# Kernel tuning notes

Measured on AMD Instinct MI355X. Metric: run time of the kernel, lower is better.

## Reference

```python
import jax, jax.numpy as jnp
import numpy as np
import math


def setup_inputs() -> dict:
    key = jax.random.key(0)
    k1, k2 = jax.random.split(key)
    N, FEATS, K = 100000, 256, 2000
    node_embs = jax.random.normal(k1, (N, FEATS), dtype=jnp.float32)
    # mask of zeros = all nodes valid (original uses -inf for invalid nodes)
    mask = jnp.zeros((N, 1), dtype=jnp.float32)
    # scorer param, uniform(-stdv, stdv) with stdv = 1/sqrt(feats), as in reset_param
    stdv = 1.0 / math.sqrt(FEATS)
    scorer = jax.random.uniform(k2, (FEATS, 1), minval=-stdv, maxval=stdv, dtype=jnp.float32)
    return {"node_embs": node_embs, "mask": mask, "scorer": scorer, "k": K}


def reference(node_embs, mask, scorer, k):
    # scores: [N,1] = (node_embs @ scorer) / sum(scorer) + mask
    scores = (node_embs @ scorer) / jnp.sum(scorer) + mask
    # top-k over flattened scores (column dim is 1, so indices == node indices)
    vals, topk_indices = jax.lax.top_k(scores.ravel(), k)
    # NOTE: original filters vals > -inf (drops masked-out picks); with a finite
    # (all-zeros) mask every selected entry passes, so shape stays static [k].
    out = jnp.take(node_embs, topk_indices, axis=0)  # [k, feats]
    return out.T  # [feats, k]
```

## Files before the change

### kernel.cpp

```cpp
#include <hip/hip_runtime.h>
#include <stdint.h>


#define NBINS 4096
#define BIN_SHIFT 20
#define CAP 4096
#define HPARTS 8

__device__ __forceinline__ uint32_t f2key(float f) {
  uint32_t b = __float_as_uint(f);
  return (b & 0x80000000u) ? ~b : (b | 0x80000000u);
}

__global__ __launch_bounds__(256) void k1_scores(
    const float* __restrict__ embs, const float* __restrict__ mask,
    const float* __restrict__ scorer, uint32_t* __restrict__ keys,
    uint32_t* __restrict__ hdr, uint32_t* __restrict__ hist, int N) {
  __shared__ float tile[32 * 132];
  __shared__ float sw[256];
  __shared__ float Ssh;
  int t = threadIdx.x;
  int r0 = blockIdx.x * 32;
  if (blockIdx.x == 0) {
    if (t < 16) hdr[t] = 0u;
    for (int i = t; i < NBINS; i += 256) hist[i] = 0u;
  }
  sw[t] = scorer[t];
  __syncthreads();
  if (t < 64) {
    double s = 0.0;
    for (int j = t; j < 256; j += 64) s += (double)sw[j];
#pragma unroll
    for (int off = 32; off >= 1; off >>= 1) s += __shfl_xor(s, off, 64);
    if (t == 0) Ssh = (float)s;
  }
  __syncthreads();
  float S = Ssh;
  int r = t >> 3, c = t & 7;
  float acc = 0.f;
  const float4* e4 = (const float4*)embs;
#pragma unroll
  for (int ch = 0; ch < 2; ++ch) {
    if (ch) __syncthreads();
#pragma unroll
    for (int m = 0; m < 4; ++m) {
      int flat = m * 256 + t;
      int rr = flat >> 5;
      int cc4 = flat & 31;
      int row = r0 + rr;
      float4 v = make_float4(0.f, 0.f, 0.f, 0.f);
      if (row < N) v = e4[(size_t)row * 64 + ch * 32 + cc4];
      float* dst = &tile[rr * 132 + cc4 * 4];
      dst[0] = v.x; dst[1] = v.y; dst[2] = v.z; dst[3] = v.w;
    }
    __syncthreads();
#pragma unroll
    for (int sl = 0; sl < 16; ++sl) {
      acc = fmaf(tile[r * 132 + c + 8 * sl], sw[ch * 128 + c + 8 * sl], acc);
    }
  }
  float m1 = acc + __shfl_xor(acc, 4, 64);
  float p1 = m1 + __shfl_xor(m1, 1, 64);
  float dot = p1 + __shfl_xor(p1, 2, 64);
  int row = r0 + r;
  if (c == 0 && row < N) {
    float score = dot / S + mask[row];
    keys[row] = f2key(score);
  }
}

__global__ __launch_bounds__(1024) void kHistFind(
    const uint32_t* __restrict__ keys, uint32_t* __restrict__ hist,
    uint32_t* __restrict__ hdr, int N, int k) {
  __shared__ uint32_t h[2][NBINS];
  __shared__ uint32_t wtot[16], wsuf[16];
  int t = threadIdx.x, bid = blockIdx.x;
  int lane = t & 63, wave = t >> 6;

  for (int i = t; i < 2 * NBINS; i += 1024) ((uint32_t*)h)[i] = 0u;
  __syncthreads();
  int per = (N + HPARTS - 1) / HPARTS;
  int lo = bid * per;
  int hi = lo + per; if (hi > N) hi = N;
  int sub = (t >> 7) & 1;
  int n4 = (hi - lo) >> 2;
  const uint4* q4 = (const uint4*)(keys + lo);
  for (int i = t; i < n4; i += 1024) {
    uint4 v = q4[i];
    atomicAdd(&h[sub][v.x >> BIN_SHIFT], 1u);
    atomicAdd(&h[sub][v.y >> BIN_SHIFT], 1u);
    atomicAdd(&h[sub][v.z >> BIN_SHIFT], 1u);
    atomicAdd(&h[sub][v.w >> BIN_SHIFT], 1u);
  }
  for (int i = lo + (n4 << 2) + t; i < hi; i += 1024)
    atomicAdd(&h[sub][keys[i] >> BIN_SHIFT], 1u);
  __syncthreads();
  for (int i = t; i < NBINS; i += 1024) {
    uint32_t v = h[0][i] + h[1][i];
    if (v) atomicAdd(&hist[i], v);
  }
  __syncthreads();
  if (t == 0) {
    __threadfence();
    __hip_atomic_fetch_add(&hdr[8], 1u, __ATOMIC_ACQ_REL, __HIP_MEMORY_SCOPE_AGENT);
  }
  if (bid != 0) return;

  if (t == 0) {
    while (__hip_atomic_load(&hdr[8], __ATOMIC_RELAXED, __HIP_MEMORY_SCOPE_AGENT) < HPARTS)
      __builtin_amdgcn_s_sleep(8);
    (void)__hip_atomic_load(&hdr[8], __ATOMIC_ACQUIRE, __HIP_MEMORY_SCOPE_AGENT);
  }
  __syncthreads();

  uint4 a = ((const uint4*)hist)[t];
  uint32_t rb[4] = {a.x, a.y, a.z, a.w};
  uint32_t p4 = rb[0] + rb[1] + rb[2] + rb[3];
  uint32_t x = p4;
#pragma unroll
  for (int off = 1; off < 64; off <<= 1) {
    uint32_t v = __shfl_down(x, off, 64);
    if (lane + off < 64) x += v;
  }
  if (lane == 0) wtot[wave] = x;
  __syncthreads();
  if (t < 16) {
    uint32_t y = wtot[t];
#pragma unroll
    for (int off = 1; off < 16; off <<= 1) {
      uint32_t v = __shfl_down(y, off, 64);
      if (t + off < 16) y += v;
    }
    wsuf[t] = y - wtot[t];
  }
  __syncthreads();
  uint32_t St = x + wsuf[wave];
  uint32_t above = St - p4;
  if (above < (uint32_t)k && St >= (uint32_t)k) {
    uint32_t cum = above;
#pragma unroll
    for (int jj = 3; jj >= 0; --jj) {
      if (cum + rb[jj] >= (uint32_t)k) { hdr[0] = (uint32_t)(t * 4 + jj); hdr[1] = cum; break; }
      cum += rb[jj];
    }
  }
}

__global__ __launch_bounds__(256) void k3_compact(
    const uint32_t* __restrict__ keys, const uint32_t* __restrict__ hdr,
    uint32_t* __restrict__ ckey, uint32_t* __restrict__ cidx,
    uint32_t* __restrict__ counter, int N) {
  __shared__ uint32_t wcnt[4];
  __shared__ uint32_t wbase[4];
  __shared__ uint32_t blkbase;
  int i = blockIdx.x * 256 + threadIdx.x;
  int wave = threadIdx.x >> 6, lane = threadIdx.x & 63;
  uint32_t B = hdr[0];
  bool pred = false;
  uint32_t key = 0;
  if (i < N) {
    key = keys[i];
    pred = (key >> BIN_SHIFT) >= B;
  }
  unsigned long long ball = __ballot(pred);
  uint32_t prefix = (uint32_t)__popcll(ball & ((1ull << lane) - 1ull));
  if (lane == 0) wcnt[wave] = (uint32_t)__popcll(ball);
  __syncthreads();
  if (threadIdx.x == 0) {
    uint32_t tot = wcnt[0] + wcnt[1] + wcnt[2] + wcnt[3];
    blkbase = tot ? atomicAdd(counter, tot) : 0u;
    wbase[0] = 0;
    wbase[1] = wcnt[0];
    wbase[2] = wcnt[0] + wcnt[1];
    wbase[3] = wcnt[0] + wcnt[1] + wcnt[2];
  }
  __syncthreads();
  if (pred) {
    uint32_t pos = blkbase + wbase[wave] + prefix;
    if (pos < CAP) { ckey[pos] = key; cidx[pos] = (uint32_t)i; }
  }
}

__global__ __launch_bounds__(256) void k4_rank(
    const uint32_t* __restrict__ ckey, const uint32_t* __restrict__ cidx,
    const uint32_t* __restrict__ hdr, uint32_t* __restrict__ oidx, int k) {
  __shared__ uint32_t lk[CAP];
  __shared__ uint32_t li[CAP];
  uint32_t C = hdr[2];
  if (C > CAP) C = CAP;
  uint32_t base = blockIdx.x * 16u;
  if (base >= C) return;
  for (uint32_t j = threadIdx.x; j < C; j += 256u) {
    lk[j] = ckey[j];
    li[j] = cidx[j];
  }
  __syncthreads();
  int wave = threadIdx.x >> 6, lane = threadIdx.x & 63;
  uint32_t g0 = base + wave * 4u;
  uint32_t mk[4], mi[4], cnt[4];
#pragma unroll
  for (int q = 0; q < 4; ++q) {
    uint32_t g = g0 + q;
    bool valid = g < C;
    mk[q] = valid ? lk[g] : 0u;
    mi[q] = valid ? li[g] : 0xFFFFFFFFu;
    cnt[q] = 0u;
  }
  for (uint32_t j = lane; j < C; j += 64u) {
    uint32_t kj = lk[j], ij = li[j];
#pragma unroll
    for (int q = 0; q < 4; ++q)
      cnt[q] += (kj > mk[q] || (kj == mk[q] && ij < mi[q])) ? 1u : 0u;
  }
#pragma unroll
  for (int q = 0; q < 4; ++q) {
#pragma unroll
    for (int off = 32; off >= 1; off >>= 1) cnt[q] += __shfl_xor(cnt[q], off, 64);
  }
  if (lane == 0) {
#pragma unroll
    for (int q = 0; q < 4; ++q) {
      uint32_t g = g0 + q;
      if (g < C && cnt[q] < (uint32_t)k) oidx[cnt[q]] = mi[q];
    }
  }
}

__global__ __launch_bounds__(256) void k5_gather(
    const float* __restrict__ embs, const uint32_t* __restrict__ oidx,
    float* __restrict__ out, int k) {
  __shared__ float tile[16 * 132];
  __shared__ uint32_t sidx[16];
  int t = threadIdx.x;
  int r0 = blockIdx.x * 16;
  int fb = blockIdx.y * 128;
  if (t < 16) sidx[t] = (r0 + t < k) ? oidx[r0 + t] : 0u;
  __syncthreads();
  const float4* e4 = (const float4*)embs;
#pragma unroll
  for (int m = 0; m < 2; ++m) {
    int flat = m * 256 + t;
    int rr = flat >> 5;
    int cc4 = flat & 31;
    float4 v = e4[(size_t)sidx[rr] * 64 + (fb >> 2) + cc4];
    float* dst = &tile[rr * 132 + cc4 * 4];
    dst[0] = v.x; dst[1] = v.y; dst[2] = v.z; dst[3] = v.w;
  }
  __syncthreads();
  int fl = t >> 1;
  int rq = t & 1;
  float v[8];
#pragma unroll
  for (int i = 0; i < 8; ++i) v[i] = tile[(rq * 8 + i) * 132 + fl];
  size_t obase = (size_t)(fb + fl) * k + r0 + rq * 8;
  if (((k & 3) == 0) && (r0 + rq * 8 + 7 < k)) {
    *(float4*)(out + obase) = make_float4(v[0], v[1], v[2], v[3]);
    *(float4*)(out + obase + 4) = make_float4(v[4], v[5], v[6], v[7]);
  } else {
#pragma unroll
    for (int i = 0; i < 8; ++i)
      if (r0 + rq * 8 + i < k) out[obase + i] = v[i];
  }
}

extern "C" void kernel_launch(void* const* d_in, const int* in_sizes, int n_in,
                              void* d_out, int out_size, void* d_ws, size_t ws_size,
                              hipStream_t stream) {
  const float* embs = (const float*)d_in[0];
  const float* mask = (const float*)d_in[1];
  const float* scorer = (const float*)d_in[2];
  int F = in_sizes[2];
  int N = in_sizes[0] / F;
  int k = out_size / F;

  uint32_t* keys = (uint32_t*)d_out;

  char* ws = (char*)d_ws;
  uint32_t* hdr = (uint32_t*)ws;
  uint32_t* hist = (uint32_t*)(ws + 1024);
  uint32_t* ckey = (uint32_t*)(ws + 1024 + NBINS * 4);
  uint32_t* cidx = ckey + CAP;
  uint32_t* oidx = cidx + CAP;

  k1_scores<<<(N + 31) / 32, 256, 0, stream>>>(embs, mask, scorer, keys, hdr, hist, N);
  kHistFind<<<HPARTS, 1024, 0, stream>>>(keys, hist, hdr, N, k);
  k3_compact<<<(N + 255) / 256, 256, 0, stream>>>(keys, hdr, ckey, cidx, &hdr[2], N);
  k4_rank<<<(CAP + 15) / 16, 256, 0, stream>>>(ckey, cidx, hdr, oidx, k);
  k5_gather<<<dim3((k + 15) / 16, 2), 256, 0, stream>>>(embs, oidx, (float*)d_out, k);
}
```

Before: 45.23 us.

## Fuse histogram/threshold kernel with compaction using grid-wide spin flag

Merges the histogram+threshold-find kernel and the compaction kernel into one launch of about 98 blocks of 1024 threads. The first 8 blocks build the histogram, block 0 finds the threshold bin and publishes it through an atomic flag, and all other blocks spin-wait on that flag before compacting their slice. This removes one kernel launch and its launch gap. It relies on every block being co-resident, otherwise spinning blocks could deadlock, and hdr[9] must be reset each call.

Result: faster. 43.28 us (median of 2 runs) (-4.3%).

```diff
diff --git a/kernel.cpp b/kernel.cpp
--- a/kernel.cpp
+++ b/kernel.cpp
@@ -69,93 +69,103 @@
   }
 }
 
-__global__ __launch_bounds__(1024) void kHistFind(
+__global__ __launch_bounds__(1024) void kSel(
     const uint32_t* __restrict__ keys, uint32_t* __restrict__ hist,
-    uint32_t* __restrict__ hdr, int N, int k) {
+    uint32_t* __restrict__ hdr, uint32_t* __restrict__ ckey,
+    uint32_t* __restrict__ cidx, int N, int k) {
   __shared__ uint32_t h[2][NBINS];
   __shared__ uint32_t wtot[16], wsuf[16];
+  __shared__ uint32_t wcnt[16], wbase[16];
+  __shared__ uint32_t blkbase;
   int t = threadIdx.x, bid = blockIdx.x;
   int lane = t & 63, wave = t >> 6;
 
-  for (int i = t; i < 2 * NBINS; i += 1024) ((uint32_t*)h)[i] = 0u;
-  __syncthreads();
-  int per = (N + HPARTS - 1) / HPARTS;
-  int lo = bid * per;
-  int hi = lo + per; if (hi > N) hi = N;
-  int sub = (t >> 7) & 1;
-  int n4 = (hi - lo) >> 2;
-  const uint4* q4 = (const uint4*)(keys + lo);
-  for (int i = t; i < n4; i += 1024) {
-    uint4 v = q4[i];
-    atomicAdd(&h[sub][v.x >> BIN_SHIFT], 1u);
-    atomicAdd(&h[sub][v.y >> BIN_SHIFT], 1u);
-    atomicAdd(&h[sub][v.z >> BIN_SHIFT], 1u);
-    atomicAdd(&h[sub][v.w >> BIN_SHIFT], 1u);
-  }
-  for (int i = lo + (n4 << 2) + t; i < hi; i += 1024)
-    atomicAdd(&h[sub][keys[i] >> BIN_SHIFT], 1u);
-  __syncthreads();
-  for (int i = t; i < NBINS; i += 1024) {
-    uint32_t v = h[0][i] + h[1][i];
-    if (v) atomicAdd(&hist[i], v);
-  }
-  __syncthreads();
-  if (t == 0) {
-    __threadfence();
-    __hip_atomic_fetch_add(&hdr[8], 1u, __ATOMIC_ACQ_REL, __HIP_MEMORY_SCOPE_AGENT);
-  }
-  if (bid != 0) return;
-
-  if (t == 0) {
-    while (__hip_atomic_load(&hdr[8], __ATOMIC_RELAXED, __HIP_MEMORY_SCOPE_AGENT) < HPARTS)
-      __builtin_amdgcn_s_sleep(8);
-    (void)__hip_atomic_load(&hdr[8], __ATOMIC_ACQUIRE, __HIP_MEMORY_SCOPE_AGENT);
-  }
-  __syncthreads();
-
-  uint4 a = ((const uint4*)hist)[t];
-  uint32_t rb[4] = {a.x, a.y, a.z, a.w};
-  uint32_t p4 = rb[0] + rb[1] + rb[2] + rb[3];
-  uint32_t x = p4;
-#pragma unroll
-  for (int off = 1; off < 64; off <<= 1) {
-    uint32_t v = __shfl_down(x, off, 64);
-    if (lane + off < 64) x += v;
-  }
-  if (lane == 0) wtot[wave] = x;
-  __syncthreads();
-  if (t < 16) {
-    uint32_t y = wtot[t];
-#pragma unroll
-    for (int off = 1; off < 16; off <<= 1) {
-      uint32_t v = __shfl_down(y, off, 64);
-      if (t + off < 16) y += v;
-    }
-    wsuf[t] = y - wtot[t];
-  }
-  __syncthreads();
-  uint32_t St = x + wsuf[wave];
-  uint32_t above = St - p4;
-  if (above < (uint32_t)k && St >= (uint32_t)k) {
-    uint32_t cum = above;
-#pragma unroll
-    for (int jj = 3; jj >= 0; --jj) {
-      if (cum + rb[jj] >= (uint32_t)k) { hdr[0] = (uint32_t)(t * 4 + jj); hdr[1] = cum; break; }
-      cum += rb[jj];
-    }
-  }
-}
-
-__global__ __launch_bounds__(256) void k3_compact(
-    const uint32_t* __restrict__ keys, const uint32_t* __restrict__ hdr,
-    uint32_t* __restrict__ ckey, uint32_t* __restrict__ cidx,
-    uint32_t* __restrict__ counter, int N) {
-  __shared__ uint32_t wcnt[4];
-  __shared__ uint32_t wbase[4];
-  __shared__ uint32_t blkbase;
-  int i = blockIdx.x * 256 + threadIdx.x;
-  int wave = threadIdx.x >> 6, lane = threadIdx.x & 63;
+  if (bid < HPARTS) {
+    for (int i = t; i < 2 * NBINS; i += 1024) ((uint32_t*)h)[i] = 0u;
+    __syncthreads();
+    int per = (N + HPARTS - 1) / HPARTS;
+    int lo = bid * per;
+    int hi = lo + per; if (hi > N) hi = N;
+    int sub = (t >> 7) & 1;
+    int n4 = (hi - lo) >> 2;
+    const uint4* q4 = (const uint4*)(keys + lo);
+    for (int i = t; i < n4; i += 1024) {
+      uint4 v = q4[i];
+      atomicAdd(&h[sub][v.x >> BIN_SHIFT], 1u);
+      atomicAdd(&h[sub][v.y >> BIN_SHIFT], 1u);
+      atomicAdd(&h[sub][v.z >> BIN_SHIFT], 1u);
+      atomicAdd(&h[sub][v.w >> BIN_SHIFT], 1u);
+    }
+    for (int i = lo + (n4 << 2) + t; i < hi; i += 1024)
+      atomicAdd(&h[sub][keys[i] >> BIN_SHIFT], 1u);
+    __syncthreads();
+    for (int i = t; i < NBINS; i += 1024) {
+      uint32_t v = h[0][i] + h[1][i];
+      if (v) atomicAdd(&hist[i], v);
+    }
+    __syncthreads();
+    if (t == 0) {
+      __threadfence();
+      __hip_atomic_fetch_add(&hdr[8], 1u, __ATOMIC_ACQ_REL, __HIP_MEMORY_SCOPE_AGENT);
+    }
+  }
+
+  if (bid == 0) {
+    if (t == 0) {
+      while (__hip_atomic_load(&hdr[8], __ATOMIC_RELAXED, __HIP_MEMORY_SCOPE_AGENT) < HPARTS)
+        __builtin_amdgcn_s_sleep(8);
+      (void)__hip_atomic_load(&hdr[8], __ATOMIC_ACQUIRE, __HIP_MEMORY_SCOPE_AGENT);
+    }
+    __syncthreads();
+    uint4 a = ((const uint4*)hist)[t];
+    uint32_t rb[4] = {a.x, a.y, a.z, a.w};
+    uint32_t p4 = rb[0] + rb[1] + rb[2] + rb[3];
+    uint32_t x = p4;
+#pragma unroll
+    for (int off = 1; off < 64; off <<= 1) {
+      uint32_t v = __shfl_down(x, off, 64);
+      if (lane + off < 64) x += v;
+    }
+    if (lane == 0) wtot[wave] = x;
+    __syncthreads();
+    if (t < 16) {
+      uint32_t y = wtot[t];
+#pragma unroll
+      for (int off = 1; off < 16; off <<= 1) {
+        uint32_t v = __shfl_down(y, off, 64);
+        if (t + off < 16) y += v;
+      }
+      wsuf[t] = y - wtot[t];
+    }
+    __syncthreads();
+    uint32_t St = x + wsuf[wave];
+    uint32_t above = St - p4;
+    if (above < (uint32_t)k && St >= (uint32_t)k) {
+      uint32_t cum = above;
+#pragma unroll
+      for (int jj = 3; jj >= 0; --jj) {
+        if (cum + rb[jj] >= (uint32_t)k) {
+          hdr[0] = (uint32_t)(t * 4 + jj);
+          hdr[1] = cum;
+          __threadfence();
+          __hip_atomic_fetch_add(&hdr[9], 1u, __ATOMIC_ACQ_REL, __HIP_MEMORY_SCOPE_AGENT);
+          break;
+        }
+        cum += rb[jj];
+      }
+    }
+    __syncthreads();
+  } else {
+    if (t == 0) {
+      while (__hip_atomic_load(&hdr[9], __ATOMIC_RELAXED, __HIP_MEMORY_SCOPE_AGENT) < 1u)
+        __builtin_amdgcn_s_sleep(16);
+      (void)__hip_atomic_load(&hdr[9], __ATOMIC_ACQUIRE, __HIP_MEMORY_SCOPE_AGENT);
+    }
+    __syncthreads();
+  }
   uint32_t B = hdr[0];
+
+  int i = bid * 1024 + t;
   bool pred = false;
   uint32_t key = 0;
   if (i < N) {
@@ -166,13 +176,11 @@
   uint32_t prefix = (uint32_t)__popcll(ball & ((1ull << lane) - 1ull));
   if (lane == 0) wcnt[wave] = (uint32_t)__popcll(ball);
   __syncthreads();
-  if (threadIdx.x == 0) {
-    uint32_t tot = wcnt[0] + wcnt[1] + wcnt[2] + wcnt[3];
-    blkbase = tot ? atomicAdd(counter, tot) : 0u;
-    wbase[0] = 0;
-    wbase[1] = wcnt[0];
-    wbase[2] = wcnt[0] + wcnt[1];
-    wbase[3] = wcnt[0] + wcnt[1] + wcnt[2];
+  if (t == 0) {
+    uint32_t tot = 0;
+#pragma unroll
+    for (int w = 0; w < 16; ++w) { wbase[w] = tot; tot += wcnt[w]; }
+    blkbase = tot ? atomicAdd(&hdr[2], tot) : 0u;
   }
   __syncthreads();
   if (pred) {
@@ -282,9 +290,9 @@
   uint32_t* cidx = ckey + CAP;
   uint32_t* oidx = cidx + CAP;
 
+  int nsel = (N + 1023) / 1024;
   k1_scores<<<(N + 31) / 32, 256, 0, stream>>>(embs, mask, scorer, keys, hdr, hist, N);
-  kHistFind<<<HPARTS, 1024, 0, stream>>>(keys, hist, hdr, N, k);
-  k3_compact<<<(N + 255) / 256, 256, 0, stream>>>(keys, hdr, ckey, cidx, &hdr[2], N);
+  kSel<<<nsel, 1024, 0, stream>>>(keys, hist, hdr, ckey, cidx, N, k);
   k4_rank<<<(CAP + 15) / 16, 256, 0, stream>>>(ckey, cidx, hdr, oidx, k);
   k5_gather<<<dim3((k + 15) / 16, 2), 256, 0, stream>>>(embs, oidx, (float*)d_out, k);
 }
```
